# Performance work log

Hardware: AMD Instinct MI355X
Metric: run time of the kernel (lower is better)

The kernel has to match this reference:

```python
import jax, jax.numpy as jnp
import numpy as np

N = 20000
E = 640000
F_IN = 128
C_T = 8
L_T = 10 * N
HEADS = 8
HDIM = 64
NEG_SLOPE = 0.2


def setup_inputs() -> dict:
    key = jax.random.key(0)
    ks = jax.random.split(key, 20)
    d = {}
    d["x"] = jax.random.normal(ks[0], (N, F_IN), dtype=jnp.float32)
    d["edge_index"] = jax.random.randint(ks[1], (2, E), 0, N, dtype=jnp.int64)
    d["temporal"] = jax.random.normal(ks[2], (C_T, L_T), dtype=jnp.float32)
    # GCNConv(F_IN, 16)
    d["W1"] = jax.random.normal(ks[3], (F_IN, 16), dtype=jnp.float32) * 0.1
    d["b1"] = jnp.zeros((16,), dtype=jnp.float32)
    # GATConv(16, 64, heads=8), concat -> 512
    d["W2"] = jax.random.normal(ks[4], (16, HEADS * HDIM), dtype=jnp.float32) * 0.1
    d["att_src"] = jax.random.normal(ks[5], (HEADS, HDIM), dtype=jnp.float32) * 0.1
    d["att_dst"] = jax.random.normal(ks[6], (HEADS, HDIM), dtype=jnp.float32) * 0.1
    d["b2"] = jnp.zeros((HEADS * HDIM,), dtype=jnp.float32)
    # TemporalCNN
    d["cw1"] = jax.random.normal(ks[7], (32, C_T, 3), dtype=jnp.float32) * 0.1
    d["cb1"] = jnp.zeros((32,), dtype=jnp.float32)
    d["cw2"] = jax.random.normal(ks[8], (64, 32, 3), dtype=jnp.float32) * 0.05
    d["cb2"] = jnp.zeros((64,), dtype=jnp.float32)
    d["cw3"] = jax.random.normal(ks[9], (128, 64, 3), dtype=jnp.float32) * 0.05
    d["cb3"] = jnp.zeros((128,), dtype=jnp.float32)
    d["fw1"] = jax.random.normal(ks[10], (256, 128 * 10), dtype=jnp.float32) * 0.02
    d["fb1"] = jnp.zeros((256,), dtype=jnp.float32)
    d["fw2"] = jax.random.normal(ks[11], (64, 256), dtype=jnp.float32) * 0.05
    d["fb2"] = jnp.zeros((64,), dtype=jnp.float32)
    return d


def _conv1d(x, w, b):
    # x: [1, C, L], w: [O, C, 3]; padding=1 == SAME for k=3
    out = jax.lax.conv_general_dilated(
        x, w, window_strides=(1,), padding="SAME",
        dimension_numbers=("NCH", "OIH", "NCH"))
    return out + b[None, :, None]


def _gcn(x, src, dst, W, b):
    # PyG GCNConv: add self-loops, symmetric normalization
    h = x @ W                                   # [N, 16]
    deg = jax.ops.segment_sum(jnp.ones_like(dst, dtype=h.dtype), dst, num_segments=N)
    dinv = jax.lax.rsqrt(jnp.maximum(deg, 1.0))
    norm = dinv[src] * dinv[dst]                # [E+N]
    out = jax.ops.segment_sum(h[src] * norm[:, None], dst, num_segments=N)
    return out + b


def _gat(x, src, dst, W, att_src, att_dst, b):
    h = (x @ W).reshape(N, HEADS, HDIM)         # [N, 8, 64]
    a_s = jnp.einsum("nhd,hd->nh", h, att_src)  # [N, 8]
    a_d = jnp.einsum("nhd,hd->nh", h, att_dst)
    e = a_s[src] + a_d[dst]                     # [E+N, 8], message j->i: src=j, dst=i
    e = jnp.where(e >= 0, e, NEG_SLOPE * e)     # LeakyReLU(0.2)
    # segment softmax over incoming edges of each dst node
    m = jax.ops.segment_max(e, dst, num_segments=N)
    m = jnp.where(jnp.isfinite(m), m, 0.0)
    ex = jnp.exp(e - m[dst])
    s = jax.ops.segment_sum(ex, dst, num_segments=N)
    alpha = ex / (s[dst] + 1e-16)               # [E+N, 8]
    out = jax.ops.segment_sum(h[src] * alpha[:, :, None], dst, num_segments=N)
    return out.reshape(N, HEADS * HDIM) + b


def reference(x, edge_index, temporal, W1, b1, W2, att_src, att_dst, b2,
              cw1, cb1, cw2, cb2, cw3, cb3, fw1, fb1, fw2, fb2):
    # ---- graph branch ----
    loops = jnp.arange(N, dtype=edge_index.dtype)
    src = jnp.concatenate([edge_index[0], loops])
    dst = jnp.concatenate([edge_index[1], loops])
    g = _gcn(x, src, dst, W1, b1)
    g = jax.nn.relu(g)
    # F.dropout with training=False (eval) -> identity
    x1 = _gat(g, src, dst, W2, att_src, att_dst, b2)   # [N, 512]
    # ---- temporal branch ----
    t = temporal[None]                                  # [1, C, L]
    t = jax.nn.relu(_conv1d(t, cw1, cb1))
    t = jax.nn.relu(_conv1d(t, cw2, cb2))
    t = jax.nn.relu(_conv1d(t, cw3, cb3))               # [1, 128, L]
    t = t.reshape(-1, 128 * 10)                         # [N, 1280] (same as torch .view)
    t = jax.nn.relu(t @ fw1.T + fb1)
    x2 = t @ fw2.T + fb2                                # [N, 64]
    return jnp.concatenate([x1, x2], axis=1)            # [N, 576]
```

## Files before the change

### kernel.cpp

```cpp
#include <hip/hip_runtime.h>
#include <hip/hip_bf16.h>

#define NN 20000
#define EE 640000
#define FIN 128
#define CT 8
#define LT 200000
#define HEADS 8
#define HDIM 64
#define F1 16
#define F2 512
#define OUTF 576

typedef short s16x8 __attribute__((ext_vector_type(8)));
typedef float f32x4 __attribute__((ext_vector_type(4)));

static __device__ __forceinline__ float b2f(__hip_bfloat16 v) { return __bfloat162float(v); }
static __device__ __forceinline__ float ldf(float v) { return v; }
static __device__ __forceinline__ float ldf(__hip_bfloat16 v) { return __bfloat162float(v); }
static __device__ __forceinline__ unsigned f2bf_bits(float x) {
  unsigned u = __float_as_uint(x);
  return (u + 0x7fffu + ((u >> 16) & 1u)) >> 16;
}


__global__ __launch_bounds__(256) void wprep_kernel(
    const float* __restrict__ cw, float* __restrict__ wt, int O, int C) {
  int i = blockIdx.x * 256 + threadIdx.x;
  if (i >= O * C * 3) return;
  int o = i / (C * 3), r = i % (C * 3);
  int c = r / 3, k = r % 3;
  wt[(c * 3 + k) * O + o] = cw[i];
}

__global__ __launch_bounds__(256) void wprep_bf(
    const float* __restrict__ cw, short* __restrict__ wb, int O, int C) {
  int i = blockIdx.x * 256 + threadIdx.x;
  if (i >= O * C * 3) return;
  int o = i / (C * 3), r = i % (C * 3);
  int ic = r / 3, kk = r % 3;
  wb[o * 3 * C + kk * C + ic] = (short)f2bf_bits(cw[i]);
}

template <int C, int O, int P, typename IN_T>
__global__ __launch_bounds__(256) void conv_fast(
    const IN_T* __restrict__ in, __hip_bfloat16* __restrict__ out,
    const float* __restrict__ wt, const float* __restrict__ bias) {
  constexpr int OCG = O / 2;
  constexpr int PG = 256 / OCG;
  static_assert(PG * P == 64, "tile mismatch");
  __shared__ __align__(16) float tile[C][68];
  __shared__ __align__(16) __hip_bfloat16 ot[O][66];
  int t = threadIdx.x;
  int ocg = t % OCG;
  int pg = t / OCG;
  long base = (long)blockIdx.x * 64;

  for (int i = t; i < C * 66; i += 256) {
    int c = i / 66, p = i % 66;
    long l = base + p - 1;
    tile[c][p] = (l >= 0 && l < LT) ? ldf(in[(long)c * LT + l]) : 0.f;
  }
  __syncthreads();

  int oc0 = 2 * ocg;
  int p0 = pg * P;
  float acc[2][P];
#pragma unroll
  for (int j = 0; j < 2; j++)
#pragma unroll
    for (int p = 0; p < P; p++) acc[j][p] = 0.f;

  for (int ic = 0; ic < C; ic++) {
    float x[P + 2];
#pragma unroll
    for (int q = 0; q < P / 4; q++) {
      float4 v = *(const float4*)&tile[ic][p0 + 4 * q];
      x[4 * q] = v.x; x[4 * q + 1] = v.y; x[4 * q + 2] = v.z; x[4 * q + 3] = v.w;
    }
    {
      float2 v = *(const float2*)&tile[ic][p0 + P];
      x[P] = v.x; x[P + 1] = v.y;
    }
    const float* wrow = wt + (long)ic * 3 * O;
    float wv[3][2];
#pragma unroll
    for (int kk = 0; kk < 3; kk++) {
      float2 w2 = *(const float2*)&wrow[kk * O + oc0];
      wv[kk][0] = w2.x; wv[kk][1] = w2.y;
    }
#pragma unroll
    for (int kk = 0; kk < 3; kk++)
#pragma unroll
      for (int j = 0; j < 2; j++)
#pragma unroll
        for (int p = 0; p < P; p++) acc[j][p] += x[p + kk] * wv[kk][j];
  }
  float b0 = bias[oc0], b1 = bias[oc0 + 1];
#pragma unroll
  for (int p = 0; p < P; p++) {
    ot[oc0][p0 + p] = __float2bfloat16(fmaxf(acc[0][p] + b0, 0.f));
    ot[oc0 + 1][p0 + p] = __float2bfloat16(fmaxf(acc[1][p] + b1, 0.f));
  }
  __syncthreads();
  for (int i = t; i < O * 32; i += 256) {
    int oc = i >> 5, pp = i & 31;
    unsigned v = ((const unsigned*)&ot[oc][0])[pp];
    *(unsigned*)&out[(long)oc * LT + base + 2 * pp] = v;
  }
}

template <int C, int O, int MPW>
__global__ __launch_bounds__(256) void conv_mfma(
    const short* __restrict__ in, short* __restrict__ out,
    const short* __restrict__ w, const float* __restrict__ bias) {
  constexpr int K = 3 * C;
  constexpr int NS = K / 32;
  constexpr int XP = C + 8;
  constexpr int OP = 132;
  constexpr int SH_X = 132 * XP * 2;
  constexpr int SH_O = O * OP * 2;
  __shared__ __align__(16) char smem[(SH_X > SH_O) ? SH_X : SH_O];
  short* xT = (short*)smem;

  int t = threadIdx.x;
  long base = (long)blockIdx.x * 128;

  for (int idx = t; idx < C * 132; idx += 256) {
    int ic = idx / 132, p = idx % 132;
    long l = base + p - 1;
    xT[p * XP + ic] = (l >= 0 && l < LT) ? in[(long)ic * LT + l] : (short)0;
  }
  __syncthreads();

  int wave = t >> 6, lane = t & 63;
  int n = lane & 15, kg = lane >> 4;
  int m0 = wave * (MPW * 16);

  f32x4 acc[MPW][8] = {};
#pragma unroll
  for (int s = 0; s < NS; s++) {
    const int kk = (s * 32) / C;
    const int ic0 = (s * 32) % C + kg * 8;
    s16x8 a[MPW];
#pragma unroll
    for (int mi = 0; mi < MPW; mi++)
      a[mi] = *(const s16x8*)(w + (long)(m0 + mi * 16 + n) * K + s * 32 + kg * 8);
#pragma unroll
    for (int nt = 0; nt < 8; nt++) {
      s16x8 b = *(const s16x8*)(xT + (nt * 16 + n + kk) * XP + ic0);
#pragma unroll
      for (int mi = 0; mi < MPW; mi++)
        acc[mi][nt] = __builtin_amdgcn_mfma_f32_16x16x32_bf16(a[mi], b, acc[mi][nt], 0, 0, 0);
    }
  }

  __syncthreads();
  short* ob = (short*)smem;
#pragma unroll
  for (int mi = 0; mi < MPW; mi++) {
    int o = m0 + mi * 16 + kg * 4;
#pragma unroll
    for (int nt = 0; nt < 8; nt++) {
      int p = nt * 16 + n;
#pragma unroll
      for (int r = 0; r < 4; r++) {
        float v = fmaxf(acc[mi][nt][r] + bias[o + r], 0.f);
        ob[(o + r) * OP + p] = (short)f2bf_bits(v);
      }
    }
  }
  __syncthreads();
  const unsigned* obu = (const unsigned*)smem;
  for (int idx = t; idx < O * 64; idx += 256) {
    int o = idx >> 6, q = idx & 63;
    long l = base + 2 * q;
    if (l < LT)
      *(unsigned*)(out + (long)o * LT + l) = obu[o * (OP / 2) + q];
  }
}

__global__ __launch_bounds__(256) void fw1bf_kernel(
    const float* __restrict__ fw1, __hip_bfloat16* __restrict__ w) {
  int i = blockIdx.x * 256 + threadIdx.x;
  if (i < 256 * 1280) w[i] = __float2bfloat16(fw1[i]);
}

__global__ __launch_bounds__(256) void fw2t_kernel(
    const float* __restrict__ fw2, float* __restrict__ fw2t) {
  int i = blockIdx.x * 256 + threadIdx.x;
  if (i >= 64 * 256) return;
  int o = i / 256, j = i % 256;
  fw2t[j * 64 + o] = fw2[i];
}

__global__ __launch_bounds__(256) void fc1_mfma(
    const __hip_bfloat16* __restrict__ t3, const __hip_bfloat16* __restrict__ w,
    const float* __restrict__ fb1, float* __restrict__ out) {
  int wave = threadIdx.x >> 6;
  int lane = threadIdx.x & 63;
  int m0 = blockIdx.x * 32;
  int n0 = wave * 64;
  int mrow = lane & 15;
  int kg = lane >> 4;
  const short* A0 = (const short*)t3 + (long)(m0 + mrow) * 1280 + kg * 8;
  const short* A1 = A0 + 16 * 1280;
  const short* B0 = (const short*)w + (long)(n0 + mrow) * 1280 + kg * 8;
  f32x4 acc[2][4] = {};
  for (int k0 = 0; k0 < 1280; k0 += 32) {
    s16x8 a0 = *(const s16x8*)(A0 + k0);
    s16x8 a1 = *(const s16x8*)(A1 + k0);
#pragma unroll
    for (int t = 0; t < 4; t++) {
      s16x8 b = *(const s16x8*)(B0 + (long)t * 16 * 1280 + k0);
      acc[0][t] = __builtin_amdgcn_mfma_f32_16x16x32_bf16(a0, b, acc[0][t], 0, 0, 0);
      acc[1][t] = __builtin_amdgcn_mfma_f32_16x16x32_bf16(a1, b, acc[1][t], 0, 0, 0);
    }
  }
  int crow = kg * 4;
#pragma unroll
  for (int t = 0; t < 4; t++) {
    int col = n0 + t * 16 + mrow;
    float bias = fb1[col];
#pragma unroll
    for (int mt = 0; mt < 2; mt++) {
#pragma unroll
      for (int r = 0; r < 4; r++) {
        int node = m0 + mt * 16 + crow + r;
        out[(long)node * 256 + col] = fmaxf(acc[mt][t][r] + bias, 0.f);
      }
    }
  }
}

__global__ __launch_bounds__(256) void fc2_kernel(
    const float* __restrict__ fc1o, const float* __restrict__ fw2t,
    const float* __restrict__ fb2, float* __restrict__ out) {
  __shared__ float sh[32][257];
  int t = threadIdx.x;
  int m0 = blockIdx.x * 32;
  for (int i = t; i < 32 * 256; i += 256) {
    int nd = i >> 8, j = i & 255;
    sh[nd][j] = fc1o[(long)(m0 + nd) * 256 + j];
  }
  __syncthreads();
  int wave = t >> 6, o = t & 63;
  int nb = wave * 8;
  float acc[8];
  float bias = fb2[o];
#pragma unroll
  for (int i = 0; i < 8; i++) acc[i] = bias;
  for (int j = 0; j < 256; j++) {
    float wv = fw2t[j * 64 + o];
#pragma unroll
    for (int i = 0; i < 8; i++) acc[i] += sh[nb + i][j] * wv;
  }
#pragma unroll
  for (int i = 0; i < 8; i++)
    out[(long)(m0 + nb + i) * OUTF + F2 + o] = acc[i];
}


__global__ __launch_bounds__(256) void zero_i32(int* __restrict__ p, int n) {
  int i = blockIdx.x * 256 + threadIdx.x;
  if (i < n) p[i] = 0;
}

__global__ __launch_bounds__(256) void deg_kernel(const int* __restrict__ dst, int* __restrict__ deg) {
  int e = blockIdx.x * 256 + threadIdx.x;
  if (e < EE) atomicAdd(&deg[dst[e]], 1);
}

__global__ __launch_bounds__(256) void dinv_kernel(const int* __restrict__ deg, float* __restrict__ dinv) {
  int i = blockIdx.x * 256 + threadIdx.x;
  if (i < NN) dinv[i] = rsqrtf((float)(deg[i] + 1));
}

__global__ __launch_bounds__(1024) void scan_kernel(const int* __restrict__ deg, int* __restrict__ offs) {
  __shared__ int sums[1024];
  int tid = threadIdx.x;
  const int CH = 20;
  int s = 0;
  for (int i = 0; i < CH; i++) {
    int idx = tid * CH + i;
    if (idx < NN) s += deg[idx] + 1;
  }
  sums[tid] = s;
  __syncthreads();
  for (int off = 1; off < 1024; off <<= 1) {
    int v = (tid >= off) ? sums[tid - off] : 0;
    __syncthreads();
    sums[tid] += v;
    __syncthreads();
  }
  int run = (tid > 0) ? sums[tid - 1] : 0;
  for (int i = 0; i < CH; i++) {
    int idx = tid * CH + i;
    if (idx < NN) {
      offs[idx] = run;
      run += deg[idx] + 1;
    }
  }
  if (tid == 1023) offs[NN] = sums[1023];
}

__global__ __launch_bounds__(256) void fill_kernel(
    const int* __restrict__ src, const int* __restrict__ dst,
    const int* __restrict__ offs, int* __restrict__ cursor, int* __restrict__ csr) {
  int e = blockIdx.x * 256 + threadIdx.x;
  if (e < EE) {
    int d = dst[e];
    int pos = atomicAdd(&cursor[d], 1);
    csr[offs[d] + pos] = src[e];
  } else if (e < EE + NN) {
    int i = e - EE;
    int pos = atomicAdd(&cursor[i], 1);
    csr[offs[i] + pos] = i;
  }
}

__global__ __launch_bounds__(256) void h1_kernel(
    const float* __restrict__ x, const float* __restrict__ W1,
    float* __restrict__ h1) {
  int idx = blockIdx.x * 256 + threadIdx.x;
  if (idx >= NN * F1) return;
  int n = idx >> 4, f = idx & 15;
  float acc = 0.f;
  for (int k = 0; k < FIN; k++) acc += x[n * FIN + k] * W1[k * F1 + f];
  h1[idx] = acc;
}

__global__ __launch_bounds__(64) void gcn_kernel(
    const float* __restrict__ h1, const int* __restrict__ offs, const int* __restrict__ csr,
    const float* __restrict__ dinv, const float* __restrict__ b1, float* __restrict__ g) {
  int i = blockIdx.x;
  int tid = threadIdx.x;
  int f = tid & 15, grp = tid >> 4;
  int beg = offs[i], end = offs[i + 1];
  float acc = 0.f;
  for (int idx = beg + grp; idx < end; idx += 4) {
    int s = csr[idx];
    acc += h1[s * F1 + f] * dinv[s];
  }
  acc += __shfl_down(acc, 32);
  acc += __shfl_down(acc, 16);
  if (tid < 16) g[i * F1 + f] = fmaxf(acc * dinv[i] + b1[f], 0.f);
}

__global__ __launch_bounds__(256) void att_prep(
    const float* __restrict__ W2, const float* __restrict__ asrc,
    const float* __restrict__ adst, float* __restrict__ WS, float* __restrict__ WD) {
  int t = threadIdx.x;
  int k = (t & 127) >> 3, h = t & 7;
  const float* av = (t < 128) ? asrc : adst;
  float acc = 0.f;
  for (int d = 0; d < 64; d++) acc += W2[k * F2 + h * 64 + d] * av[h * 64 + d];
  ((t < 128) ? WS : WD)[k * 8 + h] = acc;
}

__global__ __launch_bounds__(256) void h2att_kernel(
    const float* __restrict__ g, const float* __restrict__ W2,
    const float* __restrict__ WS, const float* __restrict__ WD,
    unsigned* __restrict__ h2hm, float* __restrict__ AS, float* __restrict__ AD) {
  __shared__ __align__(16) float gl[32][20];
  int t = threadIdx.x;
  int i0 = blockIdx.x * 32;
  for (int idx = t; idx < 512; idx += 256)
    gl[idx >> 4][idx & 15] = g[i0 * 16 + idx];
  __syncthreads();

  int f0 = 2 * t;
  int h = t >> 5, c32 = t & 31;
  float w0[16], w1[16];
#pragma unroll
  for (int k = 0; k < 16; k++) {
    float2 wv = *(const float2*)&W2[k * F2 + f0];
    w0[k] = wv.x; w1[k] = wv.y;
  }
  for (int nl = 0; nl < 32; nl++) {
    float a0 = 0.f, a1 = 0.f;
#pragma unroll
    for (int kk = 0; kk < 4; kk++) {
      f32x4 gv = *(const f32x4*)&gl[nl][4 * kk];
#pragma unroll
      for (int r = 0; r < 4; r++) {
        a0 += gv[r] * w0[4 * kk + r];
        a1 += gv[r] * w1[4 * kk + r];
      }
    }
    h2hm[((long)h * NN + i0 + nl) * 32 + c32] = f2bf_bits(a0) | (f2bf_bits(a1) << 16);
  }
  int nl = t >> 3, hh = t & 7;
  float s = 0.f, d = 0.f;
#pragma unroll
  for (int k = 0; k < 16; k++) {
    float gv = gl[nl][k];
    s += gv * WS[k * 8 + hh];
    d += gv * WD[k * 8 + hh];
  }
  AS[(long)hh * NN + i0 + nl] = s;
  AD[(long)hh * NN + i0 + nl] = d;
}

__global__ __launch_bounds__(256) void gat_fused_kernel(
    const unsigned* __restrict__ h2hm, const float* __restrict__ AS,
    const float* __restrict__ AD, const int* __restrict__ offs,
    const int* __restrict__ csr, const float* __restrict__ b2,
    float* __restrict__ out) {
  __shared__ __align__(16) unsigned long long pairs[4][64];
  __shared__ __align__(16) float accb[4][8][68];
  int h = blockIdx.x & 7;
  int gn = blockIdx.x >> 3;
  int wave = threadIdx.x >> 6;
  int lane = threadIdx.x & 63;
  int i = gn * 4 + wave;
  int beg = offs[i], end = offs[i + 1];
  const float* ASh = AS + (long)h * NN;
  float ad = AD[(long)h * NN + i];
  const char* hb2 = (const char*)(h2hm + (long)h * NN * 32);
  int octet = lane >> 3, q = lane & 7;
  unsigned laneoff = (unsigned)q * 16u;
  unsigned long long* prs = &pairs[wave][0];

  float acc[8] = {0.f, 0.f, 0.f, 0.f, 0.f, 0.f, 0.f, 0.f};
  float sum = 0.f;

  for (int c = beg; c < end; c += 64) {
    int cnt = end - c;
    if (cnt > 64) cnt = 64;
    unsigned off = 0u;
    float ex = 0.f;
    if (lane < cnt) {
      int s = csr[c + lane];
      float e = ASh[s] + ad;
      e = (e >= 0.f) ? e : 0.2f * e;
      ex = __expf(e);
      sum += ex;
      off = (unsigned)s << 7;
    }
    asm volatile("" ::: "memory");
    prs[lane] = ((unsigned long long)__float_as_uint(ex) << 32) | off;
    asm volatile("" ::: "memory");
    int nj = (cnt + 7) >> 3;
    const unsigned long long* pp = prs + octet;
#pragma unroll 2
    for (int j = 0; j < nj; j++) {
      unsigned long long pr = pp[(long)j * 8];
      unsigned voff = (unsigned)pr | laneoff;
      float aj = __uint_as_float((unsigned)(pr >> 32));
      uint4 v = *(const uint4*)(hb2 + voff);
      acc[0] += __uint_as_float(v.x << 16) * aj;
      acc[1] += __uint_as_float(v.x & 0xffff0000u) * aj;
      acc[2] += __uint_as_float(v.y << 16) * aj;
      acc[3] += __uint_as_float(v.y & 0xffff0000u) * aj;
      acc[4] += __uint_as_float(v.z << 16) * aj;
      acc[5] += __uint_as_float(v.z & 0xffff0000u) * aj;
      acc[6] += __uint_as_float(v.w << 16) * aj;
      acc[7] += __uint_as_float(v.w & 0xffff0000u) * aj;
    }
    asm volatile("" ::: "memory");
  }
#pragma unroll
  for (int o = 32; o > 0; o >>= 1) sum += __shfl_xor(sum, o, 64);
  float rinv = 1.f / (sum + 1e-16f);
  float* ab = &accb[wave][octet][q * 8];
  f32x4 lo = {acc[0], acc[1], acc[2], acc[3]};
  f32x4 hi = {acc[4], acc[5], acc[6], acc[7]};
  *(f32x4*)ab = lo;
  *(f32x4*)(ab + 4) = hi;
  asm volatile("" ::: "memory");
  float r = 0.f;
#pragma unroll
  for (int o = 0; o < 8; o++) r += accb[wave][o][lane];
  out[(long)i * OUTF + h * 64 + lane] = r * rinv + b2[h * 64 + lane];
}


extern "C" void kernel_launch(void* const* d_in, const int* in_sizes, int n_in,
                              void* d_out, int out_size, void* d_ws, size_t ws_size,
                              hipStream_t stream) {
  const float* x        = (const float*)d_in[0];
  const int*   eidx     = (const int*)d_in[1];
  const float* temporal = (const float*)d_in[2];
  const float* W1       = (const float*)d_in[3];
  const float* b1       = (const float*)d_in[4];
  const float* W2       = (const float*)d_in[5];
  const float* att_src  = (const float*)d_in[6];
  const float* att_dst  = (const float*)d_in[7];
  const float* b2       = (const float*)d_in[8];
  const float* cw1      = (const float*)d_in[9];
  const float* cb1      = (const float*)d_in[10];
  const float* cw2      = (const float*)d_in[11];
  const float* cb2      = (const float*)d_in[12];
  const float* cw3      = (const float*)d_in[13];
  const float* cb3      = (const float*)d_in[14];
  const float* fw1      = (const float*)d_in[15];
  const float* fb1      = (const float*)d_in[16];
  const float* fw2      = (const float*)d_in[17];
  const float* fb2      = (const float*)d_in[18];
  float* out = (float*)d_out;

  const int* e_src = eidx;
  const int* e_dst = eidx + EE;

  char* ws = (char*)d_ws;
  __hip_bfloat16* T1b = (__hip_bfloat16*)(ws + 0);
  __hip_bfloat16* T2b = (__hip_bfloat16*)(ws + 12800000);
  __hip_bfloat16* T3b = (__hip_bfloat16*)(ws + 38400000);
  __hip_bfloat16* FW1BF = (__hip_bfloat16*)(ws + 0);
  float* FW2T   = (float*)(ws + 655360);
  float* FC1OUT = (float*)(ws + 1310720);
  float* H1     = (float*)(ws + 0);
  float* G      = (float*)(ws + 1280000);
  int*   DEG    = (int*)  (ws + 2560000);
  float* DINV   = (float*)(ws + 2640000);
  int*   OFFS   = (int*)  (ws + 2720000);
  int*   CURSOR = (int*)  (ws + 2800128);
  int*   CSR    = (int*)  (ws + 2880128);
  float* AS     = (float*)(ws + 5520128);
  float* AD     = (float*)(ws + 6160128);
  unsigned* H2HM = (unsigned*)(ws + 6800128);
  float* WSM    = (float*)(ws + 2560000);
  float* WDM    = (float*)(ws + 2560512);
  float* WT1 = out;
  short* WB2 = (short*)((char*)d_out + 3072);
  short* WB3 = (short*)((char*)d_out + 15360);

  const int PB = LT / 64;
  const int MB = (LT + 127) / 128;

  wprep_kernel<<<(32 * 8 * 3 + 255) / 256, 256, 0, stream>>>(cw1, WT1, 32, 8);
  wprep_bf<<<(64 * 32 * 3 + 255) / 256, 256, 0, stream>>>(cw2, WB2, 64, 32);
  wprep_bf<<<(128 * 64 * 3 + 255) / 256, 256, 0, stream>>>(cw3, WB3, 128, 64);
  conv_fast<8, 32, 4, float><<<PB, 256, 0, stream>>>(temporal, T1b, WT1, cb1);
  conv_mfma<32, 64, 1><<<MB, 256, 0, stream>>>((const short*)T1b, (short*)T2b, WB2, cb2);
  fw1bf_kernel<<<(256 * 1280 + 255) / 256, 256, 0, stream>>>(fw1, FW1BF);
  fw2t_kernel<<<(64 * 256 + 255) / 256, 256, 0, stream>>>(fw2, FW2T);
  conv_mfma<64, 128, 2><<<MB, 256, 0, stream>>>((const short*)T2b, (short*)T3b, WB3, cb3);
  fc1_mfma<<<NN / 32, 256, 0, stream>>>(T3b, FW1BF, fb1, FC1OUT);
  fc2_kernel<<<NN / 32, 256, 0, stream>>>(FC1OUT, FW2T, fb2, out);

  zero_i32<<<(NN + 255) / 256, 256, 0, stream>>>(DEG, NN);
  zero_i32<<<(NN + 255) / 256, 256, 0, stream>>>(CURSOR, NN);
  deg_kernel<<<(EE + 255) / 256, 256, 0, stream>>>(e_dst, DEG);
  dinv_kernel<<<(NN + 255) / 256, 256, 0, stream>>>(DEG, DINV);
  scan_kernel<<<1, 1024, 0, stream>>>(DEG, OFFS);
  att_prep<<<1, 256, 0, stream>>>(W2, att_src, att_dst, WSM, WDM);
  fill_kernel<<<(EE + NN + 255) / 256, 256, 0, stream>>>(e_src, e_dst, OFFS, CURSOR, CSR);
  h1_kernel<<<(NN * F1 + 255) / 256, 256, 0, stream>>>(x, W1, H1);
  gcn_kernel<<<NN, 64, 0, stream>>>(H1, OFFS, CSR, DINV, b1, G);
  h2att_kernel<<<NN / 32, 256, 0, stream>>>(G, W2, WSM, WDM, H2HM, AS, AD);
  gat_fused_kernel<<<(NN / 4) * 8, 256, 0, stream>>>(H2HM, AS, AD, OFFS, CSR, b2, out);
}
```

Measured before the change: 510.5 us.

## Tile fc1 GEMM into 128x128 LDS blocks with double-buffered direct-to-LDS loads

Replaces the fc1 MFMA kernel, which read A and B straight from global memory per wave with little reuse, with a 128x128 block tile. Each K-step is staged into shared memory through global_load_lds and double-buffered so the next stage loads while the current one computes. Each wave computes a 64x64 sub-tile with 16 accumulators. This raises arithmetic intensity and cuts redundant global reads of the weights. The cost is more registers and LDS per block and fewer blocks (314), which may lower occupancy; the tail rows are clamped and masked.

Result: faster. 475.2 us (-6.9%).

```diff
diff --git a/kernel.cpp b/kernel.cpp
--- a/kernel.cpp
+++ b/kernel.cpp
@@ -21,6 +21,12 @@
 static __device__ __forceinline__ unsigned f2bf_bits(float x) {
   unsigned u = __float_as_uint(x);
   return (u + 0x7fffu + ((u >> 16) & 1u)) >> 16;
+}
+
+static __device__ __forceinline__ void gl16(const void* g, void* l) {
+  __builtin_amdgcn_global_load_lds(
+      (const __attribute__((address_space(1))) unsigned*)g,
+      (__attribute__((address_space(3))) unsigned*)l, 16, 0, 0);
 }
 
 
@@ -194,40 +200,75 @@
   fw2t[j * 64 + o] = fw2[i];
 }
 
-__global__ __launch_bounds__(256) void fc1_mfma(
+__global__ __launch_bounds__(256) void fc1_tile(
     const __hip_bfloat16* __restrict__ t3, const __hip_bfloat16* __restrict__ w,
     const float* __restrict__ fb1, float* __restrict__ out) {
-  int wave = threadIdx.x >> 6;
-  int lane = threadIdx.x & 63;
-  int m0 = blockIdx.x * 32;
-  int n0 = wave * 64;
-  int mrow = lane & 15;
-  int kg = lane >> 4;
-  const short* A0 = (const short*)t3 + (long)(m0 + mrow) * 1280 + kg * 8;
-  const short* A1 = A0 + 16 * 1280;
-  const short* B0 = (const short*)w + (long)(n0 + mrow) * 1280 + kg * 8;
-  f32x4 acc[2][4] = {};
-  for (int k0 = 0; k0 < 1280; k0 += 32) {
-    s16x8 a0 = *(const s16x8*)(A0 + k0);
-    s16x8 a1 = *(const s16x8*)(A1 + k0);
-#pragma unroll
-    for (int t = 0; t < 4; t++) {
-      s16x8 b = *(const s16x8*)(B0 + (long)t * 16 * 1280 + k0);
-      acc[0][t] = __builtin_amdgcn_mfma_f32_16x16x32_bf16(a0, b, acc[0][t], 0, 0, 0);
-      acc[1][t] = __builtin_amdgcn_mfma_f32_16x16x32_bf16(a1, b, acc[1][t], 0, 0, 0);
-    }
-  }
-  int crow = kg * 4;
-#pragma unroll
-  for (int t = 0; t < 4; t++) {
-    int col = n0 + t * 16 + mrow;
+  __shared__ __align__(16) short As[2][128 * 32];
+  __shared__ __align__(16) short Bs[2][128 * 32];
+  int t = threadIdx.x;
+  int wid = t >> 6, lane = t & 63;
+  int bn = blockIdx.x & 1, bm = blockIdx.x >> 1;
+  int mrow = lane & 15, kg = lane >> 4;
+
+  const char* tb = (const char*)t3;
+  const char* wb = (const char*)w;
+  int u0 = wid * 128 + lane;
+  int u1 = u0 + 64;
+  int ra0 = u0 >> 2, ca0 = u0 & 3;
+  int ra1 = u1 >> 2, ca1 = u1 & 3;
+  long ga0 = ((long)min(bm * 128 + ra0, NN - 1) * 1280 + ca0 * 8) * 2;
+  long ga1 = ((long)min(bm * 128 + ra1, NN - 1) * 1280 + ca1 * 8) * 2;
+  long gb0 = ((long)(bn * 128 + ra0) * 1280 + ca0 * 8) * 2;
+  long gb1 = ((long)(bn * 128 + ra1) * 1280 + ca1 * 8) * 2;
+  int l0 = (wid * 2 + 0) * 512;
+  int l1 = (wid * 2 + 1) * 512;
+
+#define FC1_STAGE(buf, k0)                          \
+  do {                                              \
+    long kb = (long)(k0) * 2;                       \
+    gl16(tb + ga0 + kb, &As[buf][l0]);              \
+    gl16(tb + ga1 + kb, &As[buf][l1]);              \
+    gl16(wb + gb0 + kb, &Bs[buf][l0]);              \
+    gl16(wb + gb1 + kb, &Bs[buf][l1]);              \
+  } while (0)
+
+  FC1_STAGE(0, 0);
+  __syncthreads();
+
+  int wr = wid >> 1, wc = wid & 1;
+  f32x4 acc[4][4] = {};
+  for (int s = 0; s < 40; s++) {
+    int buf = s & 1;
+    if (s + 1 < 40) FC1_STAGE(buf ^ 1, (s + 1) * 32);
+    s16x8 a[4], b[4];
+#pragma unroll
+    for (int mi = 0; mi < 4; mi++)
+      a[mi] = *(const s16x8*)&As[buf][(wr * 64 + mi * 16 + mrow) * 32 + kg * 8];
+#pragma unroll
+    for (int ni = 0; ni < 4; ni++)
+      b[ni] = *(const s16x8*)&Bs[buf][(wc * 64 + ni * 16 + mrow) * 32 + kg * 8];
+#pragma unroll
+    for (int mi = 0; mi < 4; mi++)
+#pragma unroll
+      for (int ni = 0; ni < 4; ni++)
+        acc[mi][ni] = __builtin_amdgcn_mfma_f32_16x16x32_bf16(a[mi], b[ni], acc[mi][ni], 0, 0, 0);
+    __syncthreads();
+  }
+#undef FC1_STAGE
+
+  int node_base = bm * 128 + wr * 64 + kg * 4;
+  int col_base = bn * 128 + wc * 64 + mrow;
+#pragma unroll
+  for (int ni = 0; ni < 4; ni++) {
+    int col = col_base + ni * 16;
     float bias = fb1[col];
 #pragma unroll
-    for (int mt = 0; mt < 2; mt++) {
+    for (int mi = 0; mi < 4; mi++) {
+      int node = node_base + mi * 16;
 #pragma unroll
       for (int r = 0; r < 4; r++) {
-        int node = m0 + mt * 16 + crow + r;
-        out[(long)node * 256 + col] = fmaxf(acc[mt][t][r] + bias, 0.f);
+        if (node + r < NN)
+          out[(long)(node + r) * 256 + col] = fmaxf(acc[mi][ni][r] + bias, 0.f);
       }
     }
   }
@@ -537,7 +578,7 @@
   fw1bf_kernel<<<(256 * 1280 + 255) / 256, 256, 0, stream>>>(fw1, FW1BF);
   fw2t_kernel<<<(64 * 256 + 255) / 256, 256, 0, stream>>>(fw2, FW2T);
   conv_mfma<64, 128, 2><<<MB, 256, 0, stream>>>((const short*)T2b, (short*)T3b, WB3, cb3);
-  fc1_mfma<<<NN / 32, 256, 0, stream>>>(T3b, FW1BF, fb1, FC1OUT);
+  fc1_tile<<<157 * 2, 256, 0, stream>>>(T3b, FW1BF, fb1, FC1OUT);
   fc2_kernel<<<NN / 32, 256, 0, stream>>>(FC1OUT, FW2T, fb2, out);
 
   zero_i32<<<(NN + 255) / 256, 256, 0, stream>>>(DEG, NN);
```
